# Kernel optimization log

Measured on AMD Instinct MI355X. Metric: run time of the kernel, lower is better.

## Reference

```python
import jax, jax.numpy as jnp
import numpy as np

B, S, H = 1, 2048, 4096
NQ, NKV = 32, 8
HD = H // NQ  # 128


def _rope_tables(seq_len, head_dim, base=10000.0):
    inv_freq = 1.0 / (base ** (np.arange(0, head_dim, 2, dtype=np.float32) / head_dim))
    t = np.arange(seq_len, dtype=np.float32)
    freqs = np.outer(t, inv_freq)  # (S, HD/2)
    emb = np.concatenate([freqs, freqs], axis=-1)  # (S, HD)
    return jnp.asarray(np.cos(emb)), jnp.asarray(np.sin(emb))


def setup_inputs() -> dict:
    key = jax.random.key(0)
    ks = jax.random.split(key, 5)
    cos, sin = _rope_tables(S, HD)
    scale = 1.0 / np.sqrt(H)
    return {
        "hidden_states": jax.random.normal(ks[0], (B, S, H), dtype=jnp.float32),
        "cos": cos,
        "sin": sin,
        "wq": jax.random.normal(ks[1], (H, NQ * HD), dtype=jnp.float32) * scale,
        "wk": jax.random.normal(ks[2], (H, NKV * HD), dtype=jnp.float32) * scale,
        "wv": jax.random.normal(ks[3], (H, NKV * HD), dtype=jnp.float32) * scale,
        "wo": jax.random.normal(ks[4], (NQ * HD, H), dtype=jnp.float32) * scale,
    }


def _rotate_half(x):
    x1, x2 = jnp.split(x, 2, axis=-1)
    return jnp.concatenate([-x2, x1], axis=-1)


def reference(hidden_states, cos, sin, wq, wk, wv, wo):
    b, s, _ = hidden_states.shape
    q = (hidden_states @ wq).reshape(b, s, NQ, HD)
    k = (hidden_states @ wk).reshape(b, s, NKV, HD)
    v = (hidden_states @ wv).reshape(b, s, NKV, HD)
    c = cos[None, :, None, :]
    sn = sin[None, :, None, :]
    q = q * c + _rotate_half(q) * sn
    k = k * c + _rotate_half(k) * sn
    groups = NQ // NKV
    # GQA: compute scores per kv-head group without materially repeating K/V beyond einsum
    q = q.reshape(b, s, NKV, groups, HD)
    # scores: (b, kv_head, group, s_q, s_k)
    scores = jnp.einsum("bqhgd,bkhd->bhgqk", q, k) / jnp.sqrt(jnp.asarray(HD, q.dtype))
    causal = jnp.tril(jnp.ones((s, s), dtype=bool))
    scores = jnp.where(causal[None, None, None], scores, jnp.finfo(scores.dtype).min)
    attn = jax.nn.softmax(scores, axis=-1)
    out = jnp.einsum("bhgqk,bkhd->bqhgd", attn, v)  # (b, s, kv_h, g, d)
    out = out.reshape(b, s, NQ * HD)
    return out @ wo
```

## Files before the change

kernel.cpp:

```cpp
#include <hip/hip_runtime.h>
#include <hip/hip_bf16.h>
#include <math.h>

#define S_LEN 2048
#define HDIM  4096
#define NQ_H  32
#define NKV_H 8
#define HD_   128
#define DQ (NQ_H*HD_)
#define DKV (NKV_H*HD_)
#define NFUSE (DQ + 2*DKV)

typedef unsigned short u16;
typedef unsigned int   u32;
typedef __attribute__((ext_vector_type(8))) short short8;
typedef __attribute__((ext_vector_type(4))) float f32x4;

__device__ __forceinline__ u16 bf16_rne(float x) {
    u32 u = __float_as_uint(x);
    u = (u + 0x7FFFu + ((u >> 16) & 1u)) >> 16;
    return (u16)u;
}
__device__ __forceinline__ float bf16_to_f(u16 h) {
    return __uint_as_float(((u32)h) << 16);
}
__device__ __forceinline__ void glds16(const u16* g, u16* l) {
    __builtin_amdgcn_global_load_lds(
        (const __attribute__((address_space(1))) u32*)g,
        (__attribute__((address_space(3))) u32*)l,
        16, 0, 0);
}

__global__ __launch_bounds__(256) void cvt_bf16(const float* __restrict__ in,
                                                u16* __restrict__ out, int n) {
    int i = (blockIdx.x * 256 + threadIdx.x) * 8;
    if (i >= n) return;
    float4 a = *(const float4*)&in[i];
    float4 b = *(const float4*)&in[i + 4];
    u16 h[8];
    h[0] = bf16_rne(a.x); h[1] = bf16_rne(a.y); h[2] = bf16_rne(a.z); h[3] = bf16_rne(a.w);
    h[4] = bf16_rne(b.x); h[5] = bf16_rne(b.y); h[6] = bf16_rne(b.z); h[7] = bf16_rne(b.w);
    *(uint4*)&out[i] = *(uint4*)h;
}

__global__ __launch_bounds__(256) void cvtT_qkv(const float* __restrict__ wq,
                                                const float* __restrict__ wk,
                                                const float* __restrict__ wv,
                                                u16* __restrict__ WT) {
    __shared__ float tile[32][33];
    const int n0g = blockIdx.x * 32;
    const int k0  = blockIdx.y * 32;
    const float* W; int Nsrc, nloc0;
    if (n0g < DQ)            { W = wq; Nsrc = DQ;  nloc0 = n0g; }
    else if (n0g < DQ + DKV) { W = wk; Nsrc = DKV; nloc0 = n0g - DQ; }
    else                     { W = wv; Nsrc = DKV; nloc0 = n0g - DQ - DKV; }
    const int tx = threadIdx.x & 31;
    const int ty = threadIdx.x >> 5;
#pragma unroll
    for (int i = 0; i < 4; ++i)
        tile[ty + 8 * i][tx] = W[(size_t)(k0 + ty + 8 * i) * Nsrc + nloc0 + tx];
    __syncthreads();
#pragma unroll
    for (int i = 0; i < 4; ++i) {
        int r = ty + 8 * i;
        WT[(size_t)(n0g + r) * HDIM + k0 + tx] = bf16_rne(tile[tx][r]);
    }
}

__global__ __launch_bounds__(256) void cvtT(const float* __restrict__ W,
                                            u16* __restrict__ WT, int K, int N) {
    __shared__ float tile[32][33];
    const int n0 = blockIdx.x * 32;
    const int k0 = blockIdx.y * 32;
    const int tx = threadIdx.x & 31;
    const int ty = threadIdx.x >> 5;
#pragma unroll
    for (int i = 0; i < 4; ++i)
        tile[ty + 8 * i][tx] = W[(size_t)(k0 + ty + 8 * i) * N + n0 + tx];
    __syncthreads();
#pragma unroll
    for (int i = 0; i < 4; ++i) {
        int r = ty + 8 * i;
        WT[(size_t)(n0 + r) * K + k0 + tx] = bf16_rne(tile[tx][r]);
    }
}

#define AOFFU(par, mh) ((par) * 16384 + (mh) * 8192)
#define BOFFU(par, nh) (32768 + (par) * 16384 + (nh) * 8192)

__global__ __launch_bounds__(512, 2) void gemm_qkv256(const u16* __restrict__ A,
                                                      const u16* __restrict__ BT,
                                                      u16* __restrict__ qb,
                                                      u16* __restrict__ kb,
                                                      u16* __restrict__ vb) {
    const int K  = HDIM;
    const int NT = K / 64;
    __shared__ u16 smem[65536] __attribute__((aligned(16)));

    const int t    = threadIdx.x;
    const int w    = t >> 6;
    const int lane = t & 63;
    const int wm   = w >> 2;
    const int wn   = w & 3;
    const int fr   = lane & 15;
    const int quad = lane >> 4;
    const int m0   = blockIdx.y * 256;
    const int n0   = blockIdx.x * 256;

    const int lrow = lane >> 3;
    const int lc   = (lane & 7) ^ lrow;
    const u16* const baseA = A  + (size_t)(m0 + w * 16 + lrow) * K + lc * 8;
    const u16* const baseB = BT + (size_t)(n0 + w * 16 + lrow) * K + lc * 8;
    const int wdst = w * 1024;

    const int pc0  = (quad ^ (fr & 7)) * 8;
    const int pc1  = pc0 ^ 32;
    const int aRow = (wm * 64 + fr) * 64;
    const int bRow = (wn * 32 + fr) * 64;

    f32x4 acc[2][2][4][2];
#pragma unroll
    for (int a = 0; a < 2; ++a)
#pragma unroll
        for (int b = 0; b < 2; ++b)
#pragma unroll
            for (int c = 0; c < 4; ++c)
#pragma unroll
                for (int d = 0; d < 2; ++d) acc[a][b][c][d] = (f32x4)0.f;

    short8 ar0[4][2], ar1[4][2], br[2][2];

    auto stA = [&](int off, int tile, int mh) {
        const u16* g = baseA + (size_t)mh * 128 * K + tile * 64;
        glds16(g,                 smem + off + wdst);
        glds16(g + (size_t)8 * K, smem + off + wdst + 512);
    };
    auto stB = [&](int off, int tile, int nh) {
        const u16* g = baseB + (size_t)nh * 128 * K + tile * 64;
        glds16(g,                 smem + off + wdst);
        glds16(g + (size_t)8 * K, smem + off + wdst + 512);
    };
    auto rdA = [&](short8 (&d)[4][2], int off) {
#pragma unroll
        for (int mr = 0; mr < 4; ++mr) {
            d[mr][0] = *(const short8*)&smem[off + aRow + mr * 1024 + pc0];
            d[mr][1] = *(const short8*)&smem[off + aRow + mr * 1024 + pc1];
        }
    };
    auto rdB = [&](short8 (&d)[2][2], int off) {
#pragma unroll
        for (int nc = 0; nc < 2; ++nc) {
            d[nc][0] = *(const short8*)&smem[off + bRow + nc * 1024 + pc0];
            d[nc][1] = *(const short8*)&smem[off + bRow + nc * 1024 + pc1];
        }
    };
    auto mma = [&](short8 (&a)[4][2], short8 (&b)[2][2], f32x4 (&c)[4][2]) {
        __builtin_amdgcn_s_setprio(1);
#pragma unroll
        for (int mr = 0; mr < 4; ++mr)
#pragma unroll
            for (int nc = 0; nc < 2; ++nc) {
                c[mr][nc] = __builtin_amdgcn_mfma_f32_16x16x32_bf16(a[mr][0], b[nc][0], c[mr][nc], 0, 0, 0);
                c[mr][nc] = __builtin_amdgcn_mfma_f32_16x16x32_bf16(a[mr][1], b[nc][1], c[mr][nc], 0, 0, 0);
            }
        __builtin_amdgcn_s_setprio(0);
    };

    stA(AOFFU(0,0), 0, 0);
    stB(BOFFU(0,0), 0, 0);
    stA(AOFFU(0,1), 0, 1);
    stB(BOFFU(0,1), 0, 1);
    stA(AOFFU(1,0), 1, 0);
    stB(BOFFU(1,0), 1, 0);
    stA(AOFFU(1,1), 1, 1);
    asm volatile("s_waitcnt vmcnt(6)" ::: "memory");
    __builtin_amdgcn_s_barrier();

    for (int T = 0; T < NT; T += 2) {
        const int ts2 = (T + 2 < NT) ? T + 2 : NT - 1;
        const int ts3 = (T + 3 < NT) ? T + 3 : NT - 1;
        rdA(ar0, AOFFU(0,0));
        rdB(br,  BOFFU(0,0));
        stB(BOFFU(1,1), T + 1, 1);
        __builtin_amdgcn_s_barrier();
        asm volatile("s_waitcnt lgkmcnt(0)" ::: "memory");
        mma(ar0, br, acc[0][0]);
        __builtin_amdgcn_s_barrier();
        rdA(ar1, AOFFU(0,1));
        stA(AOFFU(0,0), ts2, 0);
        __builtin_amdgcn_s_barrier();
        asm volatile("s_waitcnt lgkmcnt(0)" ::: "memory");
        mma(ar1, br, acc[1][0]);
        __builtin_amdgcn_s_barrier();
        rdB(br, BOFFU(0,1));
        stB(BOFFU(0,0), ts2, 0);
        __builtin_amdgcn_s_barrier();
        asm volatile("s_waitcnt lgkmcnt(0)" ::: "memory");
        mma(ar1, br, acc[1][1]);
        __builtin_amdgcn_s_barrier();
        stA(AOFFU(0,1), ts2, 1);
        __builtin_amdgcn_s_barrier();
        asm volatile("s_waitcnt lgkmcnt(0)" ::: "memory");
        mma(ar0, br, acc[0][1]);
        asm volatile("s_waitcnt vmcnt(6)" ::: "memory");
        __builtin_amdgcn_s_barrier();
        rdA(ar0, AOFFU(1,0));
        rdB(br,  BOFFU(1,0));
        stB(BOFFU(0,1), ts2, 1);
        __builtin_amdgcn_s_barrier();
        asm volatile("s_waitcnt lgkmcnt(0)" ::: "memory");
        mma(ar0, br, acc[0][0]);
        __builtin_amdgcn_s_barrier();
        rdA(ar1, AOFFU(1,1));
        stA(AOFFU(1,0), ts3, 0);
        __builtin_amdgcn_s_barrier();
        asm volatile("s_waitcnt lgkmcnt(0)" ::: "memory");
        mma(ar1, br, acc[1][0]);
        __builtin_amdgcn_s_barrier();
        rdB(br, BOFFU(1,1));
        stB(BOFFU(1,0), ts3, 0);
        __builtin_amdgcn_s_barrier();
        asm volatile("s_waitcnt lgkmcnt(0)" ::: "memory");
        mma(ar1, br, acc[1][1]);
        __builtin_amdgcn_s_barrier();
        stA(AOFFU(1,1), ts3, 1);
        __builtin_amdgcn_s_barrier();
        asm volatile("s_waitcnt lgkmcnt(0)" ::: "memory");
        mma(ar0, br, acc[0][1]);
        asm volatile("s_waitcnt vmcnt(6)" ::: "memory");
        __builtin_amdgcn_s_barrier();
    }

    u16* dst; int stride, nbase;
    if (n0 < DQ)            { dst = qb; stride = DQ;  nbase = n0; }
    else if (n0 < DQ + DKV) { dst = kb; stride = DKV; nbase = n0 - DQ; }
    else                    { dst = vb; stride = DKV; nbase = n0 - DQ - DKV; }

    const int col = lane & 15;
    const int rq  = (lane >> 4) * 4;
#pragma unroll
    for (int mh = 0; mh < 2; ++mh)
#pragma unroll
        for (int nh = 0; nh < 2; ++nh)
#pragma unroll
            for (int mr = 0; mr < 4; ++mr)
#pragma unroll
                for (int nc = 0; nc < 2; ++nc)
#pragma unroll
                    for (int i = 0; i < 4; ++i)
                        dst[(size_t)(m0 + mh * 128 + wm * 64 + mr * 16 + rq + i) * stride
                            + nbase + nh * 128 + wn * 32 + nc * 16 + col] =
                            bf16_rne(acc[mh][nh][mr][nc][i]);
}

__global__ __launch_bounds__(256) void gemm_out(const u16* __restrict__ A,
                                                const u16* __restrict__ BT,
                                                float* __restrict__ C,
                                                int M, int N, int K) {
    __shared__ u16 sm[2 * 128 * 32] __attribute__((aligned(16)));
    u16* sA = sm;
    u16* sB = sm + 4096;

    const int t    = threadIdx.x;
    const int w    = t >> 6;
    const int lane = t & 63;
    const int m0   = blockIdx.y * 128;
    const int n0   = blockIdx.x * 128;
    const int wr   = (w >> 1) * 64;
    const int wc   = (w & 1) * 64;

    f32x4 acc[4][4];
#pragma unroll
    for (int i = 0; i < 4; ++i)
#pragma unroll
        for (int j = 0; j < 4; ++j) acc[i][j] = (f32x4)0.f;

    const int srow = lane >> 2;
    const size_t aOff = (size_t)(m0 + 32 * w + srow) * K + (size_t)(lane & 3) * 8;
    const size_t bOff = (size_t)(n0 + 32 * w + srow) * K + (size_t)(lane & 3) * 8;
    const size_t rowStep = (size_t)16 * K;
    u16* const ldsA = sA + 1024 * w;
    u16* const ldsB = sB + 1024 * w;

    const int fr = lane & 15;
    const int fq = (lane >> 4) * 8;

    for (int k0 = 0; k0 < K; k0 += 32) {
#pragma unroll
        for (int i = 0; i < 2; ++i) {
            glds16(A  + aOff + k0 + i * rowStep, ldsA + 512 * i);
            glds16(BT + bOff + k0 + i * rowStep, ldsB + 512 * i);
        }
        __syncthreads();
        short8 af[4], bf[4];
#pragma unroll
        for (int mt = 0; mt < 4; ++mt)
            af[mt] = *(const short8*)&sA[(wr + mt * 16 + fr) * 32 + fq];
#pragma unroll
        for (int nt = 0; nt < 4; ++nt)
            bf[nt] = *(const short8*)&sB[(wc + nt * 16 + fr) * 32 + fq];
#pragma unroll
        for (int mt = 0; mt < 4; ++mt)
#pragma unroll
            for (int nt = 0; nt < 4; ++nt)
                acc[mt][nt] = __builtin_amdgcn_mfma_f32_16x16x32_bf16(af[mt], bf[nt], acc[mt][nt], 0, 0, 0);
        __syncthreads();
    }

    const int col = lane & 15;
    const int rq  = (lane >> 4) * 4;
#pragma unroll
    for (int mt = 0; mt < 4; ++mt)
#pragma unroll
        for (int nt = 0; nt < 4; ++nt)
#pragma unroll
            for (int i = 0; i < 4; ++i)
                C[(size_t)(m0 + wr + mt * 16 + rq + i) * N + n0 + wc + nt * 16 + col] = acc[mt][nt][i];
}

__global__ __launch_bounds__(256) void rope2(u16* __restrict__ q, u16* __restrict__ k,
                                             const float* __restrict__ cosT,
                                             const float* __restrict__ sinT) {
    int idx = blockIdx.x * 256 + threadIdx.x;
    int d4   = (idx & 15) * 4;
    int rest = idx >> 4;
    int head = rest % (NQ_H + NKV_H);
    int s    = rest / (NQ_H + NKV_H);
    u16* base = (head < NQ_H)
        ? q + ((size_t)s * NQ_H + head) * HD_
        : k + ((size_t)s * NKV_H + (head - NQ_H)) * HD_;
    float4 c  = *(const float4*)&cosT[s * HD_ + d4];
    float4 sn = *(const float4*)&sinT[s * HD_ + d4];
    u16 lo[4], hi[4];
    *(uint2*)lo = *(uint2*)&base[d4];
    *(uint2*)hi = *(uint2*)&base[d4 + 64];
    float cs[4] = {c.x, c.y, c.z, c.w};
    float ss[4] = {sn.x, sn.y, sn.z, sn.w};
    u16 nlo[4], nhi[4];
#pragma unroll
    for (int j = 0; j < 4; ++j) {
        float x1 = bf16_to_f(lo[j]);
        float x2 = bf16_to_f(hi[j]);
        nlo[j] = bf16_rne(x1 * cs[j] - x2 * ss[j]);
        nhi[j] = bf16_rne(x2 * cs[j] + x1 * ss[j]);
    }
    *(uint2*)&base[d4]      = *(uint2*)nlo;
    *(uint2*)&base[d4 + 64] = *(uint2*)nhi;
}

__global__ __launch_bounds__(256) void transpose_v(const u16* __restrict__ V,
                                                   u16* __restrict__ Vt) {
    __shared__ u16 tile[64][72];
    const int s0  = blockIdx.x * 64;
    const int kvh = blockIdx.y >> 1;
    const int d0  = (blockIdx.y & 1) * 64;
    const int t = threadIdx.x;
    const int chunk = t & 7;
    const int row   = t >> 3;
#pragma unroll
    for (int p = 0; p < 2; ++p) {
        int s = row + 32 * p;
        uint4 x = *(const uint4*)&V[(size_t)(s0 + s) * DKV + kvh * HD_ + d0 + chunk * 8];
        *(uint4*)&tile[s][chunk * 8] = x;
    }
    __syncthreads();
#pragma unroll
    for (int p = 0; p < 2; ++p) {
        int d = row + 32 * p;
        u16 tmp[8];
#pragma unroll
        for (int j = 0; j < 8; ++j) tmp[j] = tile[chunk * 8 + j][d];
        *(uint4*)&Vt[(size_t)(kvh * HD_ + d0 + d) * S_LEN + s0 + chunk * 8] = *(uint4*)tmp;
    }
}

#define QSTR 136
#define PSTR 76
__global__ __launch_bounds__(512, 4) void attn_mfma(const u16* __restrict__ Q,
                                                    const u16* __restrict__ K,
                                                    const u16* __restrict__ Vt,
                                                    u16* __restrict__ O) {
    __shared__ u16 smem[26112] __attribute__((aligned(16)));
    u16* sK  = smem;
    u16* sVt = smem + 8192;
    u16* sP  = smem + 16384;
    u16* sQ  = sVt;

    const int id  = blockIdx.x;
    const int h   = id & 31;
    const int qt  = (id < 256) ? (15 - (id >> 5)) : ((id - 256) >> 5);
    const int kvh = h >> 2;
    const int q0  = qt * 128;
    const int t    = threadIdx.x;
    const int w    = t >> 6;
    const int lane = t & 63;
    const int fr   = lane & 15;
    const int quad = lane >> 4;
    const int nkt  = 2 * qt + 2;

    const float K1 = 0.12751744154f;
    const float K2 = 11.5415603267f;

    const int kRow  = t >> 3;
    const int kC    = t & 7;
    const int kLds0 = kRow * 128 + (((2 * kC + 0) ^ (kRow & 7)) * 8);
    const int kLds1 = kRow * 128 + (((2 * kC + 1) ^ (kRow & 7)) * 8);
    const u16* const kGp = K + (size_t)kRow * DKV + (size_t)kvh * HD_ + kC * 16;

    const int vRow  = t >> 2;
    const int vC    = t & 3;
    const int vLds0 = vRow * 64 + (((2 * vC + 0) ^ (vRow & 7)) * 8);
    const int vLds1 = vRow * 64 + (((2 * vC + 1) ^ (vRow & 7)) * 8);
    const u16* const vGp = Vt + ((size_t)kvh * HD_ + vRow) * S_LEN + vC * 16;

    uint4 kr0 = *(const uint4*)(kGp);
    uint4 kr1 = *(const uint4*)(kGp + 8);
    uint4 vr0 = *(const uint4*)(vGp);
    uint4 vr1 = *(const uint4*)(vGp + 8);

    {
        const int col  = t & 15;
        const int row4 = t >> 4;
#pragma unroll
        for (int p = 0; p < 4; ++p) {
            int row = row4 + 32 * p;
            uint4 xv = *(const uint4*)&Q[(size_t)(q0 + row) * DQ + h * HD_ + col * 8];
            *(uint4*)&sQ[row * QSTR + col * 8] = xv;
        }
    }
    __syncthreads();

    short8 aq[4];
#pragma unroll
    for (int ks = 0; ks < 4; ++ks)
        aq[ks] = *(const short8*)&sQ[(16 * w + fr) * QSTR + ks * 32 + quad * 8];

    float lrow[4] = {0.f, 0.f, 0.f, 0.f};
    f32x4 oacc[8];
#pragma unroll
    for (int n8 = 0; n8 < 8; ++n8) oacc[n8] = (f32x4)0.f;

    u16* const sPw   = sP + w * (16 * PSTR);
    const int  qwTop = q0 + 16 * w;

    for (int kt = 0; kt < nkt; ++kt) {
        const int k0 = kt * 64;
        __syncthreads();

        *(uint4*)&sK[kLds0]  = kr0;
        *(uint4*)&sK[kLds1]  = kr1;
        *(uint4*)&sVt[vLds0] = vr0;
        *(uint4*)&sVt[vLds1] = vr1;
        if (kt + 1 < nkt) {
            const u16* kp = kGp + (size_t)(k0 + 64) * DKV;
            kr0 = *(const uint4*)(kp);
            kr1 = *(const uint4*)(kp + 8);
            const u16* vp = vGp + (k0 + 64);
            vr0 = *(const uint4*)(vp);
            vr1 = *(const uint4*)(vp + 8);
        }
        __syncthreads();

        if (k0 <= qwTop + 15) {
            f32x4 sacc[4];
#pragma unroll
            for (int nt = 0; nt < 4; ++nt) sacc[nt] = (f32x4)0.f;
#pragma unroll
            for (int ks = 0; ks < 4; ++ks)
#pragma unroll
                for (int nt = 0; nt < 4; ++nt) {
                    const short8 bk = *(const short8*)
                        &sK[(nt * 16 + fr) * 128 + (((ks * 4 + quad) ^ (fr & 7)) * 8)];
                    sacc[nt] = __builtin_amdgcn_mfma_f32_16x16x32_bf16(aq[ks], bk, sacc[nt], 0, 0, 0);
                }

            if (k0 + 63 > qwTop) {
#pragma unroll
                for (int nt = 0; nt < 4; ++nt) {
                    int key = k0 + nt * 16 + fr;
#pragma unroll
                    for (int i = 0; i < 4; ++i)
                        if (key > qwTop + quad * 4 + i) sacc[nt][i] = -INFINITY;
                }
            }

#pragma unroll
            for (int nt = 0; nt < 4; ++nt)
#pragma unroll
                for (int i = 0; i < 4; ++i) {
                    float p = __builtin_amdgcn_exp2f(fmaf(sacc[nt][i], K1, -K2));
                    lrow[i] += p;
                    sPw[(quad * 4 + i) * PSTR + nt * 16 + fr] = bf16_rne(p);
                }

#pragma unroll
            for (int ks2 = 0; ks2 < 2; ++ks2) {
                const short8 ap = *(const short8*)&sPw[fr * PSTR + ks2 * 32 + quad * 8];
#pragma unroll
                for (int n8 = 0; n8 < 8; ++n8) {
                    const short8 bv = *(const short8*)
                        &sVt[(n8 * 16 + fr) * 64 + (((ks2 * 4 + quad) ^ (fr & 7)) * 8)];
                    oacc[n8] = __builtin_amdgcn_mfma_f32_16x16x32_bf16(ap, bv, oacc[n8], 0, 0, 0);
                }
            }
        }
    }

#pragma unroll
    for (int i = 0; i < 4; ++i) {
        lrow[i] += __shfl_xor(lrow[i], 1);
        lrow[i] += __shfl_xor(lrow[i], 2);
        lrow[i] += __shfl_xor(lrow[i], 4);
        lrow[i] += __shfl_xor(lrow[i], 8);
    }
#pragma unroll
    for (int i = 0; i < 4; ++i) {
        float inv = 1.f / lrow[i];
        size_t base = (size_t)(qwTop + quad * 4 + i) * DQ + h * HD_;
#pragma unroll
        for (int n8 = 0; n8 < 8; ++n8)
            O[base + n8 * 16 + fr] = bf16_rne(oacc[n8][i] * inv);
    }
}

extern "C" void kernel_launch(void* const* d_in, const int* in_sizes, int n_in,
                              void* d_out, int out_size, void* d_ws, size_t ws_size,
                              hipStream_t stream) {
    const float* X    = (const float*)d_in[0];
    const float* cosT = (const float*)d_in[1];
    const float* sinT = (const float*)d_in[2];
    const float* wq   = (const float*)d_in[3];
    const float* wk   = (const float*)d_in[4];
    const float* wv   = (const float*)d_in[5];
    const float* wo   = (const float*)d_in[6];
    float* out = (float*)d_out;

    const size_t SDQ  = (size_t)S_LEN * DQ;
    const size_t SDKV = (size_t)S_LEN * DKV;
    const size_t WQKV = (size_t)HDIM * NFUSE;

    u16* Xb  = (u16*)d_ws;
    u16* qb  = Xb + SDQ;
    u16* kb  = qb + SDQ;
    u16* vb  = kb + SDKV;
    u16* vtb = vb + SDKV;
    u16* aob = vtb + SDKV;
    u16* WT  = aob + SDQ;
    u16* woT = WT + WQKV;

    dim3 blk(256);

    cvt_bf16<<<SDQ / 2048, blk, 0, stream>>>(X, Xb, (int)SDQ);
    cvtT_qkv<<<dim3(NFUSE / 32, HDIM / 32), blk, 0, stream>>>(wq, wk, wv, WT);
    cvtT<<<dim3(HDIM / 32, DQ / 32), blk, 0, stream>>>(wo, woT, DQ, HDIM);

    gemm_qkv256<<<dim3(NFUSE / 256, S_LEN / 256), dim3(512), 0, stream>>>(Xb, WT, qb, kb, vb);

    rope2<<<(S_LEN * (NQ_H + NKV_H) * 16) / 256, blk, 0, stream>>>(qb, kb, cosT, sinT);

    transpose_v<<<dim3(S_LEN / 64, NKV_H * 2), blk, 0, stream>>>(vb, vtb);

    attn_mfma<<<dim3(512), dim3(512), 0, stream>>>(qb, kb, vtb, aob);

    gemm_out<<<dim3(HDIM / 128, S_LEN / 128), blk, 0, stream>>>(aob, woT, out, S_LEN, HDIM, DQ);
}
```

Before: 500.3 us.

## Replace output GEMM with 256x256 pipelined split-K kernel plus reduction

Replaces the simple 128x128 output projection GEMM with a 256x256-tile, 512-thread kernel. The new kernel uses swizzled LDS, a multi-stage global_load_lds pipeline, and s_setprio around the MFMA blocks, reusing the structure of the QKV GEMM. K is split in two across blockIdx.z so there are enough blocks. The second partial goes to a workspace buffer that aliases Xb/qb, which are dead by this point, and an extra add kernel sums the partials. This costs an extra launch and extra fp32 read/write traffic for the reduction.

```diff
diff --git a/kernel.cpp b/kernel.cpp
--- a/kernel.cpp
+++ b/kernel.cpp
@@ -41,6 +41,16 @@
     h[0] = bf16_rne(a.x); h[1] = bf16_rne(a.y); h[2] = bf16_rne(a.z); h[3] = bf16_rne(a.w);
     h[4] = bf16_rne(b.x); h[5] = bf16_rne(b.y); h[6] = bf16_rne(b.z); h[7] = bf16_rne(b.w);
     *(uint4*)&out[i] = *(uint4*)h;
+}
+
+__global__ __launch_bounds__(256) void add_f32(const float* __restrict__ p1,
+                                               float* __restrict__ out, int n) {
+    int i = (blockIdx.x * 256 + threadIdx.x) * 4;
+    if (i >= n) return;
+    float4 a = *(const float4*)&out[i];
+    float4 b = *(const float4*)&p1[i];
+    a.x += b.x; a.y += b.y; a.z += b.z; a.w += b.w;
+    *(float4*)&out[i] = a;
 }
 
 __global__ __launch_bounds__(256) void cvtT_qkv(const float* __restrict__ wq,
@@ -253,69 +263,165 @@
                             bf16_rne(acc[mh][nh][mr][nc][i]);
 }
 
-__global__ __launch_bounds__(256) void gemm_out(const u16* __restrict__ A,
-                                                const u16* __restrict__ BT,
-                                                float* __restrict__ C,
-                                                int M, int N, int K) {
-    __shared__ u16 sm[2 * 128 * 32] __attribute__((aligned(16)));
-    u16* sA = sm;
-    u16* sB = sm + 4096;
+__global__ __launch_bounds__(512, 2) void gemm_out256(const u16* __restrict__ A,
+                                                      const u16* __restrict__ BT,
+                                                      float* __restrict__ C,
+                                                      float* __restrict__ P1) {
+    const int LDA = DQ;
+    const int NT  = 32;
+    __shared__ u16 smem[65536] __attribute__((aligned(16)));
 
     const int t    = threadIdx.x;
     const int w    = t >> 6;
     const int lane = t & 63;
-    const int m0   = blockIdx.y * 128;
-    const int n0   = blockIdx.x * 128;
-    const int wr   = (w >> 1) * 64;
-    const int wc   = (w & 1) * 64;
-
-    f32x4 acc[4][4];
-#pragma unroll
-    for (int i = 0; i < 4; ++i)
-#pragma unroll
-        for (int j = 0; j < 4; ++j) acc[i][j] = (f32x4)0.f;
-
-    const int srow = lane >> 2;
-    const size_t aOff = (size_t)(m0 + 32 * w + srow) * K + (size_t)(lane & 3) * 8;
-    const size_t bOff = (size_t)(n0 + 32 * w + srow) * K + (size_t)(lane & 3) * 8;
-    const size_t rowStep = (size_t)16 * K;
-    u16* const ldsA = sA + 1024 * w;
-    u16* const ldsB = sB + 1024 * w;
-
-    const int fr = lane & 15;
-    const int fq = (lane >> 4) * 8;
-
-    for (int k0 = 0; k0 < K; k0 += 32) {
-#pragma unroll
-        for (int i = 0; i < 2; ++i) {
-            glds16(A  + aOff + k0 + i * rowStep, ldsA + 512 * i);
-            glds16(BT + bOff + k0 + i * rowStep, ldsB + 512 * i);
+    const int wm   = w >> 2;
+    const int wn   = w & 3;
+    const int fr   = lane & 15;
+    const int quad = lane >> 4;
+    const int m0   = blockIdx.y * 256;
+    const int n0   = blockIdx.x * 256;
+    const int kz   = blockIdx.z * 2048;
+
+    const int lrow = lane >> 3;
+    const int lc   = (lane & 7) ^ lrow;
+    const u16* const baseA = A  + (size_t)(m0 + w * 16 + lrow) * LDA + kz + lc * 8;
+    const u16* const baseB = BT + (size_t)(n0 + w * 16 + lrow) * LDA + kz + lc * 8;
+    const int wdst = w * 1024;
+
+    const int pc0  = (quad ^ (fr & 7)) * 8;
+    const int pc1  = pc0 ^ 32;
+    const int aRow = (wm * 64 + fr) * 64;
+    const int bRow = (wn * 32 + fr) * 64;
+
+    f32x4 acc[2][2][4][2];
+#pragma unroll
+    for (int a = 0; a < 2; ++a)
+#pragma unroll
+        for (int b = 0; b < 2; ++b)
+#pragma unroll
+            for (int c = 0; c < 4; ++c)
+#pragma unroll
+                for (int d = 0; d < 2; ++d) acc[a][b][c][d] = (f32x4)0.f;
+
+    short8 ar0[4][2], ar1[4][2], br[2][2];
+
+    auto stA = [&](int off, int tile, int mh) {
+        const u16* g = baseA + (size_t)mh * 128 * LDA + tile * 64;
+        glds16(g,                   smem + off + wdst);
+        glds16(g + (size_t)8 * LDA, smem + off + wdst + 512);
+    };
+    auto stB = [&](int off, int tile, int nh) {
+        const u16* g = baseB + (size_t)nh * 128 * LDA + tile * 64;
+        glds16(g,                   smem + off + wdst);
+        glds16(g + (size_t)8 * LDA, smem + off + wdst + 512);
+    };
+    auto rdA = [&](short8 (&d)[4][2], int off) {
+#pragma unroll
+        for (int mr = 0; mr < 4; ++mr) {
+            d[mr][0] = *(const short8*)&smem[off + aRow + mr * 1024 + pc0];
+            d[mr][1] = *(const short8*)&smem[off + aRow + mr * 1024 + pc1];
         }
-        __syncthreads();
-        short8 af[4], bf[4];
-#pragma unroll
-        for (int mt = 0; mt < 4; ++mt)
-            af[mt] = *(const short8*)&sA[(wr + mt * 16 + fr) * 32 + fq];
-#pragma unroll
-        for (int nt = 0; nt < 4; ++nt)
-            bf[nt] = *(const short8*)&sB[(wc + nt * 16 + fr) * 32 + fq];
-#pragma unroll
-        for (int mt = 0; mt < 4; ++mt)
-#pragma unroll
-            for (int nt = 0; nt < 4; ++nt)
-                acc[mt][nt] = __builtin_amdgcn_mfma_f32_16x16x32_bf16(af[mt], bf[nt], acc[mt][nt], 0, 0, 0);
-        __syncthreads();
-    }
-
+    };
+    auto rdB = [&](short8 (&d)[2][2], int off) {
+#pragma unroll
+        for (int nc = 0; nc < 2; ++nc) {
+            d[nc][0] = *(const short8*)&smem[off + bRow + nc * 1024 + pc0];
+            d[nc][1] = *(const short8*)&smem[off + bRow + nc * 1024 + pc1];
+        }
+    };
+    auto mma = [&](short8 (&a)[4][2], short8 (&b)[2][2], f32x4 (&c)[4][2]) {
+        __builtin_amdgcn_s_setprio(1);
+#pragma unroll
+        for (int mr = 0; mr < 4; ++mr)
+#pragma unroll
+            for (int nc = 0; nc < 2; ++nc) {
+                c[mr][nc] = __builtin_amdgcn_mfma_f32_16x16x32_bf16(a[mr][0], b[nc][0], c[mr][nc], 0, 0, 0);
+                c[mr][nc] = __builtin_amdgcn_mfma_f32_16x16x32_bf16(a[mr][1], b[nc][1], c[mr][nc], 0, 0, 0);
+            }
+        __builtin_amdgcn_s_setprio(0);
+    };
+
+    stA(AOFFU(0,0), 0, 0);
+    stB(BOFFU(0,0), 0, 0);
+    stA(AOFFU(0,1), 0, 1);
+    stB(BOFFU(0,1), 0, 1);
+    stA(AOFFU(1,0), 1, 0);
+    stB(BOFFU(1,0), 1, 0);
+    stA(AOFFU(1,1), 1, 1);
+    asm volatile("s_waitcnt vmcnt(6)" ::: "memory");
+    __builtin_amdgcn_s_barrier();
+
+    for (int T = 0; T < NT; T += 2) {
+        const int ts2 = (T + 2 < NT) ? T + 2 : NT - 1;
+        const int ts3 = (T + 3 < NT) ? T + 3 : NT - 1;
+        rdA(ar0, AOFFU(0,0));
+        rdB(br,  BOFFU(0,0));
+        stB(BOFFU(1,1), T + 1, 1);
+        __builtin_amdgcn_s_barrier();
+        asm volatile("s_waitcnt lgkmcnt(0)" ::: "memory");
+        mma(ar0, br, acc[0][0]);
+        __builtin_amdgcn_s_barrier();
+        rdA(ar1, AOFFU(0,1));
+        stA(AOFFU(0,0), ts2, 0);
+        __builtin_amdgcn_s_barrier();
+        asm volatile("s_waitcnt lgkmcnt(0)" ::: "memory");
+        mma(ar1, br, acc[1][0]);
+        __builtin_amdgcn_s_barrier();
+        rdB(br, BOFFU(0,1));
+        stB(BOFFU(0,0), ts2, 0);
+        __builtin_amdgcn_s_barrier();
+        asm volatile("s_waitcnt lgkmcnt(0)" ::: "memory");
+        mma(ar1, br, acc[1][1]);
+        __builtin_amdgcn_s_barrier();
+        stA(AOFFU(0,1), ts2, 1);
+        __builtin_amdgcn_s_barrier();
+        asm volatile("s_waitcnt lgkmcnt(0)" ::: "memory");
+        mma(ar0, br, acc[0][1]);
+        asm volatile("s_waitcnt vmcnt(6)" ::: "memory");
+        __builtin_amdgcn_s_barrier();
+        rdA(ar0, AOFFU(1,0));
+        rdB(br,  BOFFU(1,0));
+        stB(BOFFU(0,1), ts2, 1);
+        __builtin_amdgcn_s_barrier();
+        asm volatile("s_waitcnt lgkmcnt(0)" ::: "memory");
+        mma(ar0, br, acc[0][0]);
+        __builtin_amdgcn_s_barrier();
+        rdA(ar1, AOFFU(1,1));
+        stA(AOFFU(1,0), ts3, 0);
+        __builtin_amdgcn_s_barrier();
+        asm volatile("s_waitcnt lgkmcnt(0)" ::: "memory");
+        mma(ar1, br, acc[1][0]);
+        __builtin_amdgcn_s_barrier();
+        rdB(br, BOFFU(1,1));
+        stB(BOFFU(1,0), ts3, 0);
+        __builtin_amdgcn_s_barrier();
+        asm volatile("s_waitcnt lgkmcnt(0)" ::: "memory");
+        mma(ar1, br, acc[1][1]);
+        __builtin_amdgcn_s_barrier();
+        stA(AOFFU(1,1), ts3, 1);
+        __builtin_amdgcn_s_barrier();
+        asm volatile("s_waitcnt lgkmcnt(0)" ::: "memory");
+        mma(ar0, br, acc[0][1]);
+        asm volatile("s_waitcnt vmcnt(6)" ::: "memory");
+        __builtin_amdgcn_s_barrier();
+    }
+
+    float* const dst = (blockIdx.z == 0) ? C : P1;
     const int col = lane & 15;
     const int rq  = (lane >> 4) * 4;
 #pragma unroll
-    for (int mt = 0; mt < 4; ++mt)
-#pragma unroll
-        for (int nt = 0; nt < 4; ++nt)
-#pragma unroll
-            for (int i = 0; i < 4; ++i)
-                C[(size_t)(m0 + wr + mt * 16 + rq + i) * N + n0 + wc + nt * 16 + col] = acc[mt][nt][i];
+    for (int mh = 0; mh < 2; ++mh)
+#pragma unroll
+        for (int nh = 0; nh < 2; ++nh)
+#pragma unroll
+            for (int mr = 0; mr < 4; ++mr)
+#pragma unroll
+                for (int nc = 0; nc < 2; ++nc)
+#pragma unroll
+                    for (int i = 0; i < 4; ++i)
+                        dst[(size_t)(m0 + mh * 128 + wm * 64 + mr * 16 + rq + i) * HDIM
+                            + n0 + nh * 128 + wn * 32 + nc * 16 + col] =
+                            acc[mh][nh][mr][nc][i];
 }
 
 __global__ __launch_bounds__(256) void rope2(u16* __restrict__ q, u16* __restrict__ k,
@@ -548,6 +654,8 @@
     u16* WT  = aob + SDQ;
     u16* woT = WT + WQKV;
 
+    float* P1 = (float*)d_ws;
+
     dim3 blk(256);
 
     cvt_bf16<<<SDQ / 2048, blk, 0, stream>>>(X, Xb, (int)SDQ);
@@ -562,5 +670,6 @@
 
     attn_mfma<<<dim3(512), dim3(512), 0, stream>>>(qb, kb, vtb, aob);
 
-    gemm_out<<<dim3(HDIM / 128, S_LEN / 128), blk, 0, stream>>>(aob, woT, out, S_LEN, HDIM, DQ);
-}
+    gemm_out256<<<dim3(HDIM / 256, S_LEN / 256, 2), dim3(512), 0, stream>>>(aob, woT, out, P1);
+    add_f32<<<(S_LEN * HDIM) / 1024, blk, 0, stream>>>(P1, out, S_LEN * HDIM);
+}
```

After: 476.2 us. 1.05x faster.
